# Performance work log

Measured on AMD Instinct MI355X. Metric: run time of the kernel, lower is better.

Reference implementation:

```python
import jax, jax.numpy as jnp
import numpy as np

# 17 predefined bone groups indexing into the 16 bones (ragged sizes 2/3/4)
LIMBS = [[0, 1, 2], [3, 4, 5], [6, 7], [8, 9], [10, 11, 12], [13, 14, 15],
         [6, 7, 1, 2], [6, 7, 4, 5], [6, 7, 11, 12], [6, 7, 14, 15], [6, 7, 9],
         [14, 15, 11, 12], [1, 2, 4, 5], [14, 15, 4, 5], [11, 12, 4, 5],
         [10, 0], [13, 3]]
N_GROUPS = 17
MAXL = 4          # max group size; ragged groups padded to this
C = 3             # xyz coordinates per bone
HIDDEN = 16       # mlp_hidden_dim default


def _padded_indices():
    idx = np.zeros((N_GROUPS, MAXL), np.int32)
    rowmask = np.zeros((N_GROUPS, MAXL * C), np.float32)  # mask over flattened (limb, coord)
    for g, limbs in enumerate(LIMBS):
        idx[g, :len(limbs)] = limbs
        rowmask[g, :len(limbs) * C] = 1.0
    return idx, rowmask


def setup_inputs() -> dict:
    key = jax.random.key(0)
    k_x, k_w1, k_b1, k_w2, k_b2 = jax.random.split(key, 5)
    B, T = 2048, 243
    x = jax.random.normal(k_x, (B, T, 16, C), dtype=jnp.float32)
    idx_np, rowmask_np = _padded_indices()
    # per-group MLP params, stacked over the 17 groups
    W1 = jax.random.normal(k_w1, (N_GROUPS, MAXL * C, HIDDEN), jnp.float32) * 0.1
    # zero the weight rows that correspond to padded (absent) limbs ->
    # identical math to the original ragged per-group Linear(n*3, hidden)
    W1 = W1 * jnp.asarray(rowmask_np)[:, :, None]
    b1 = jax.random.normal(k_b1, (N_GROUPS, HIDDEN), jnp.float32) * 0.1
    W2 = jax.random.normal(k_w2, (N_GROUPS, HIDDEN, C), jnp.float32) * 0.1
    b2 = jax.random.normal(k_b2, (N_GROUPS, C), jnp.float32) * 0.1
    return {"x": x, "W1": W1, "b1": b1, "W2": W2, "b2": b2,
            "idx": jnp.asarray(idx_np)}


def reference(x, W1, b1, W2, b2, idx):
    B, T, J, Cc = x.shape
    # gather all 17 groups at once: [B, T, 17, MAXL, C]
    g = x[:, :, idx, :]
    g = g.reshape(B, T, N_GROUPS, MAXL * Cc)        # flatten limbs*coords per group
    # batched small GEMMs across the 17 groups (fused per-group BoneMLP)
    h = jax.nn.relu(jnp.einsum('btgi,gih->btgh', g, W1) + b1)  # [B,T,17,HIDDEN]
    out = jnp.einsum('btgh,ghc->btgc', h, W2) + b2             # [B,T,17,3]
    return out
```

## Files before the change

kernel.cpp:

```cpp
#include <hip/hip_runtime.h>


#define NG   17
#define MAXL 4
#define PITCH 257

static constexpr int KL[NG][MAXL] = {
    {0,1,2,0},   {3,4,5,0},   {6,7,0,0},   {8,9,0,0},
    {10,11,12,0},{13,14,15,0},{6,7,1,2},   {6,7,4,5},
    {6,7,11,12}, {6,7,14,15}, {6,7,9,0},   {14,15,11,12},
    {1,2,4,5},   {14,15,4,5}, {11,12,4,5}, {10,0,0,0},
    {13,3,0,0}
};

__global__ __launch_bounds__(256, 3)
void bone_kernel(const float* __restrict__ x,
                 const float* __restrict__ W1,
                 const float* __restrict__ b1,
                 const float* __restrict__ W2,
                 const float* __restrict__ b2,
                 float* __restrict__ out)
{
    __shared__ float lds[51 * PITCH];
    const int tid = threadIdx.x;
    const long long blk = blockIdx.x;

    const float4* xin = reinterpret_cast<const float4*>(x + blk * (256LL * 48));
    #pragma unroll
    for (int it = 0; it < 12; ++it) {
        const int f4  = it * 256 + tid;
        const float4 v = xin[f4];
        const int pos = f4 / 12;
        const int e0  = (f4 % 12) * 4;
        lds[(e0 + 0) * PITCH + pos] = v.x;
        lds[(e0 + 1) * PITCH + pos] = v.y;
        lds[(e0 + 2) * PITCH + pos] = v.z;
        lds[(e0 + 3) * PITCH + pos] = v.w;
    }
    __syncthreads();

    float xr[48];
    #pragma unroll
    for (int e = 0; e < 48; ++e) xr[e] = lds[e * PITCH + tid];
    __syncthreads();

    #pragma unroll
    for (int g = 0; g < NG; ++g) {
        float h[16];
        #pragma unroll
        for (int j = 0; j < 16; ++j) h[j] = b1[g * 16 + j];

        #pragma unroll
        for (int s = 0; s < MAXL; ++s) {
            const int limb = KL[g][s];
            #pragma unroll
            for (int c = 0; c < 3; ++c) {
                const float xv = xr[limb * 3 + c];
                const int   i  = s * 3 + c;
                #pragma unroll
                for (int j = 0; j < 16; ++j)
                    h[j] = fmaf(xv, W1[g * 192 + i * 16 + j], h[j]);
            }
        }
        #pragma unroll
        for (int j = 0; j < 16; ++j) h[j] = fmaxf(h[j], 0.0f);

        #pragma unroll
        for (int c = 0; c < 3; ++c) {
            float acc = b2[g * 3 + c];
            #pragma unroll
            for (int j = 0; j < 16; ++j)
                acc = fmaf(h[j], W2[g * 48 + j * 3 + c], acc);
            lds[(g * 3 + c) * PITCH + tid] = acc;
        }
    }
    __syncthreads();

    float* o = out + blk * (256LL * 51);
    for (int it = 0; it < 51; ++it) {
        const int f   = it * 256 + tid;
        const int pos = f / 51;
        const int e   = f % 51;
        o[f] = lds[e * PITCH + pos];
    }
}

extern "C" void kernel_launch(void* const* d_in, const int* in_sizes, int n_in,
                              void* d_out, int out_size, void* d_ws, size_t ws_size,
                              hipStream_t stream)
{
    const float* x  = (const float*)d_in[0];
    const float* W1 = (const float*)d_in[1];
    const float* b1 = (const float*)d_in[2];
    const float* W2 = (const float*)d_in[3];
    const float* b2 = (const float*)d_in[4];
    float* out = (float*)d_out;

    bone_kernel<<<1944, 256, 0, stream>>>(x, W1, b1, W2, b2, out);
}
```

Measured before the change: 273.5 us.

## Drop LDS transpose staging; load and store rows directly per thread

Each thread now reads its own 48-float row straight from global memory with float4 loads and writes its 51 outputs directly, instead of staging through a transposed LDS buffer with barriers. This removes the LDS traffic, the three syncthreads and the LDS-limited occupancy, and the launch-bounds occupancy hint is dropped. In exchange, global accesses become strided across lanes (192-byte stride on loads, 204-byte on scalar stores), so coalescing gets worse and the kernel leans on the caches to merge the traffic.

Result: slower. 307.7 us (+12.5%).

```diff
diff --git a/kernel.cpp b/kernel.cpp
--- a/kernel.cpp
+++ b/kernel.cpp
@@ -3,7 +3,6 @@
 
 #define NG   17
 #define MAXL 4
-#define PITCH 257
 
 static constexpr int KL[NG][MAXL] = {
     {0,1,2,0},   {3,4,5,0},   {6,7,0,0},   {8,9,0,0},
@@ -13,7 +12,7 @@
     {13,3,0,0}
 };
 
-__global__ __launch_bounds__(256, 3)
+__global__ __launch_bounds__(256)
 void bone_kernel(const float* __restrict__ x,
                  const float* __restrict__ W1,
                  const float* __restrict__ b1,
@@ -21,28 +20,20 @@
                  const float* __restrict__ b2,
                  float* __restrict__ out)
 {
-    __shared__ float lds[51 * PITCH];
-    const int tid = threadIdx.x;
-    const long long blk = blockIdx.x;
+    const long long pos = (long long)blockIdx.x * 256 + threadIdx.x;
 
-    const float4* xin = reinterpret_cast<const float4*>(x + blk * (256LL * 48));
-    #pragma unroll
-    for (int it = 0; it < 12; ++it) {
-        const int f4  = it * 256 + tid;
-        const float4 v = xin[f4];
-        const int pos = f4 / 12;
-        const int e0  = (f4 % 12) * 4;
-        lds[(e0 + 0) * PITCH + pos] = v.x;
-        lds[(e0 + 1) * PITCH + pos] = v.y;
-        lds[(e0 + 2) * PITCH + pos] = v.z;
-        lds[(e0 + 3) * PITCH + pos] = v.w;
-    }
-    __syncthreads();
-
+    const float4* xin = reinterpret_cast<const float4*>(x + pos * 48);
     float xr[48];
     #pragma unroll
-    for (int e = 0; e < 48; ++e) xr[e] = lds[e * PITCH + tid];
-    __syncthreads();
+    for (int i = 0; i < 12; ++i) {
+        const float4 v = xin[i];
+        xr[i * 4 + 0] = v.x;
+        xr[i * 4 + 1] = v.y;
+        xr[i * 4 + 2] = v.z;
+        xr[i * 4 + 3] = v.w;
+    }
+
+    float* o = out + pos * 51;
 
     #pragma unroll
     for (int g = 0; g < NG; ++g) {
@@ -71,17 +62,8 @@
             #pragma unroll
             for (int j = 0; j < 16; ++j)
                 acc = fmaf(h[j], W2[g * 48 + j * 3 + c], acc);
-            lds[(g * 3 + c) * PITCH + tid] = acc;
+            o[g * 3 + c] = acc;
         }
-    }
-    __syncthreads();
-
-    float* o = out + blk * (256LL * 51);
-    for (int it = 0; it < 51; ++it) {
-        const int f   = it * 256 + tid;
-        const int pos = f / 51;
-        const int e   = f % 51;
-        o[f] = lds[e * PITCH + pos];
     }
 }
 
```
